# Kernel tuning notes

Hardware: AMD Instinct MI355X
Metric: run time of the kernel (lower is better)

## Reference

```python
import jax, jax.numpy as jnp
import numpy as np

Q_INTERVAL = 4          # opt.interval
Q = 2 ** Q_INTERVAL     # 16, quantization bin width
L = 2 ** (8 - Q_INTERVAL) + 1  # 17, LUT side length
OUT_C = 3
BD = 1                  # padding for mode 's'


def setup_inputs() -> dict:
    key = jax.random.key(0)
    k_img, k_w = jax.random.split(key)
    # 8-bit pixel values stored as float32 (the torch module does // and % on floats)
    img_in = jax.random.randint(k_img, (8, 1, 513, 513), 0, 256).astype(jnp.float32)
    # LUT parameter, stored as float in [-1, 1] (npy / 127.0 in the original)
    weight = jax.random.uniform(k_w, (L ** 4, OUT_C), dtype=jnp.float32,
                                minval=-1.0, maxval=1.0)
    return {"img_in": img_in, "weight": weight}


def _interp_s(img_in, weight):
    """Mode 's' quadrilinear (4-simplex) LUT interpolation, faithful to
    SWF2LUT.InterpTorchBatch. The 24 explicit permutation cases in the torch
    code are exactly the descending sort of the four fractional parts
    (ties broken toward the later pixel: d before c before b before a)."""
    # weight quantization: round to int levels in [-127, 127]
    w = jnp.clip(jnp.round(weight * 127.0), -127.0, 127.0)

    h = img_in.shape[2] - BD
    ww = img_in.shape[3] - BD
    # 2x2 neighborhood (mode 's')
    a = img_in[:, :, 0:h,     0:ww]
    b = img_in[:, :, 0:h,     1:1 + ww]
    c = img_in[:, :, 1:1 + h, 0:ww]
    d = img_in[:, :, 1:1 + h, 1:1 + ww]

    ia = jnp.floor_divide(a, Q).astype(jnp.int32)
    ib = jnp.floor_divide(b, Q).astype(jnp.int32)
    ic = jnp.floor_divide(c, Q).astype(jnp.int32)
    idd = jnp.floor_divide(d, Q).astype(jnp.int32)

    f = jnp.stack([a % Q, b % Q, c % Q, d % Q], axis=-1)  # (B,C,h,w,4)

    # Descending sort with ties broken so that larger index (d,c,b,a) comes
    # first -- matches the strict '>' case ordering of the torch code.
    tie_key = f * 4.0 + jnp.arange(4, dtype=f.dtype)
    order = jnp.argsort(-tie_key, axis=-1)                 # (B,C,h,w,4)
    fs = jnp.take_along_axis(f, order, axis=-1)            # sorted desc

    strides = jnp.array([L ** 3, L ** 2, L, 1], dtype=jnp.int32)
    base = ia * (L ** 3) + ib * (L ** 2) + ic * L + idd    # (B,C,h,w)
    sstrides = strides[order]                              # (B,C,h,w,4)
    cum = jnp.cumsum(sstrides, axis=-1)
    # 5 simplex vertices: base, then incrementally add strides in sort order
    idx = jnp.concatenate([base[..., None], base[..., None] + cum], axis=-1)

    p = w[idx]                                             # (B,C,h,w,5,outC)
    wts = jnp.stack([Q - fs[..., 0],
                     fs[..., 0] - fs[..., 1],
                     fs[..., 1] - fs[..., 2],
                     fs[..., 2] - fs[..., 3],
                     fs[..., 3]], axis=-1)                 # (B,C,h,w,5)
    out = jnp.sum(wts[..., None] * p, axis=-2) / Q         # (B,C,h,w,outC)
    return out


def reference(img_in, weight):
    return _interp_s(img_in, weight)
```

## Files before the change

kernel.cpp:

```cpp
#include <hip/hip_runtime.h>
#include <stdint.h>


#define LQ   17
#define L2C  (17 * 17)
#define L3C  (17 * 17 * 17)
#define NENT (L3C * 17)
#define PLANE_STRIDE 83584
#define LDS_BYTES 83584
#define SUMSTRIDE (L3C + L2C + LQ + 1)

__device__ __forceinline__ int stride_of(int j) {
    return j == 0 ? L3C : (j == 1 ? L2C : (j == 2 ? LQ : 1));
}

__global__ __launch_bounds__(256) void quant_planar_kernel(
    const float* __restrict__ w, char* __restrict__ planes, int n) {
    int e = blockIdx.x * 256 + threadIdx.x;
    if (e >= n) return;
#pragma unroll
    for (int ch = 0; ch < 3; ++ch) {
        int q = (int)rintf(w[e * 3 + ch] * 127.0f);
        q = min(127, max(-127, q));
        planes[ch * PLANE_STRIDE + e] = (char)q;
    }
}

extern __shared__ char lut[];

__global__ __launch_bounds__(1024) void interp_fused_kernel(
    const float* __restrict__ img, const char* __restrict__ planes,
    float* __restrict__ out) {
    int G = blockIdx.x * 1024 + threadIdx.x;
    int x0 = (G & 127) << 2;
    int y  = (G >> 7) & 511;
    int im = G >> 16;

    const float* r0 = img + im * (513 * 513) + y * 513 + x0;
    const float* r1 = r0 + 513;
    float v0[5], v1[5];
#pragma unroll
    for (int i = 0; i < 5; ++i) { v0[i] = r0[i]; v1[i] = r1[i]; }

    int pi0[4], pi1[4], pi2[4], pi3[4], pfs[4];
#pragma unroll
    for (int i = 0; i < 4; ++i) {
        int a = (int)v0[i], b = (int)v0[i + 1];
        int c = (int)v1[i], d = (int)v1[i + 1];
        int base = (a >> 4) * L3C + (b >> 4) * L2C + (c >> 4) * LQ + (d >> 4);
        int k0 = ((a & 15) << 2) | 0;
        int k1 = ((b & 15) << 2) | 1;
        int k2 = ((c & 15) << 2) | 2;
        int k3 = ((d & 15) << 2) | 3;
        int t;
        if (k0 < k1) { t = k0; k0 = k1; k1 = t; }
        if (k2 < k3) { t = k2; k2 = k3; k3 = t; }
        if (k0 < k2) { t = k0; k0 = k2; k2 = t; }
        if (k1 < k3) { t = k1; k1 = k3; k3 = t; }
        if (k1 < k2) { t = k1; k1 = k2; k2 = t; }
        int fs0 = k0 >> 2, fs1 = k1 >> 2, fs2 = k2 >> 2, fs3 = k3 >> 2;
        int s0 = stride_of(k0 & 3);
        int s1 = stride_of(k1 & 3);
        int s2 = stride_of(k2 & 3);
        pi0[i] = base;
        pi1[i] = base + s0;
        pi2[i] = base + s0 + s1;
        pi3[i] = base + s0 + s1 + s2;
        pfs[i] = (fs0 << 12) | (fs1 << 8) | (fs2 << 4) | fs3;
    }

    float res[12];
#pragma unroll
    for (int ch = 0; ch < 3; ++ch) {
        __syncthreads();
        {
            const uint4* src =
                (const uint4*)(planes + (size_t)ch * PLANE_STRIDE);
            uint4* dst = (uint4*)lut;
            for (int k = threadIdx.x; k < PLANE_STRIDE / 16; k += 1024)
                dst[k] = src[k];
        }
        __syncthreads();
        const signed char* t8 = (const signed char*)lut;
#pragma unroll
        for (int i = 0; i < 4; ++i) {
            int fs = pfs[i];
            int fs0 = (fs >> 12) & 15, fs1 = (fs >> 8) & 15;
            int fs2 = (fs >> 4) & 15,  fs3 = fs & 15;
            int p0 = t8[pi0[i]];
            int p1 = t8[pi1[i]];
            int p2 = t8[pi2[i]];
            int p3 = t8[pi3[i]];
            int p4 = t8[pi0[i] + SUMSTRIDE];
            int acc = (16 - fs0) * p0 + (fs0 - fs1) * p1 + (fs1 - fs2) * p2 +
                      (fs2 - fs3) * p3 + fs3 * p4;
            res[i * 3 + ch] = (float)acc * 0.0625f;
        }
    }

    int opix = ((im * 512 + y) * 512 + x0) * 3;
    float4* o = (float4*)(out + opix);
    o[0] = make_float4(res[0], res[1], res[2], res[3]);
    o[1] = make_float4(res[4], res[5], res[6], res[7]);
    o[2] = make_float4(res[8], res[9], res[10], res[11]);
}

__global__ __launch_bounds__(256) void quant_pack_kernel(
    const float* __restrict__ w, uint32_t* __restrict__ tab, int n) {
    int e = blockIdx.x * 256 + threadIdx.x;
    if (e >= n) return;
    int q0 = (int)rintf(w[e * 3 + 0] * 127.0f);
    int q1 = (int)rintf(w[e * 3 + 1] * 127.0f);
    int q2 = (int)rintf(w[e * 3 + 2] * 127.0f);
    q0 = min(127, max(-127, q0));
    q1 = min(127, max(-127, q1));
    q2 = min(127, max(-127, q2));
    tab[e] = (uint32_t)(q0 & 0xFF) | ((uint32_t)(q1 & 0xFF) << 8) |
             ((uint32_t)(q2 & 0xFF) << 16);
}

__global__ __launch_bounds__(256) void interp_packed_kernel(
    const float* __restrict__ img, const uint32_t* __restrict__ tab,
    float* __restrict__ out) {
    int gid = blockIdx.x * 256 + threadIdx.x;
    int x0 = (gid & 127) << 2;
    int y  = (gid >> 7) & 511;
    int im = gid >> 16;

    const float* r0 = img + im * (513 * 513) + y * 513 + x0;
    const float* r1 = r0 + 513;
    float v0[5], v1[5];
#pragma unroll
    for (int i = 0; i < 5; ++i) { v0[i] = r0[i]; v1[i] = r1[i]; }

    float res[12];
#pragma unroll
    for (int i = 0; i < 4; ++i) {
        int a = (int)v0[i], b = (int)v0[i + 1];
        int c = (int)v1[i], d = (int)v1[i + 1];
        int base = (a >> 4) * L3C + (b >> 4) * L2C + (c >> 4) * LQ + (d >> 4);
        int k0 = ((a & 15) << 2) | 0;
        int k1 = ((b & 15) << 2) | 1;
        int k2 = ((c & 15) << 2) | 2;
        int k3 = ((d & 15) << 2) | 3;
        int t;
        if (k0 < k1) { t = k0; k0 = k1; k1 = t; }
        if (k2 < k3) { t = k2; k2 = k3; k3 = t; }
        if (k0 < k2) { t = k0; k0 = k2; k2 = t; }
        if (k1 < k3) { t = k1; k1 = k3; k3 = t; }
        if (k1 < k2) { t = k1; k1 = k2; k2 = t; }
        int fs0 = k0 >> 2, fs1 = k1 >> 2, fs2 = k2 >> 2, fs3 = k3 >> 2;
        int s0 = stride_of(k0 & 3);
        int s1 = stride_of(k1 & 3);
        int s2 = stride_of(k2 & 3);
        int i0 = base;
        int i1 = base + s0;
        int i2 = i1 + s1;
        int i3 = i2 + s2;
        int i4 = base + SUMSTRIDE;
        uint32_t u0 = tab[i0], u1 = tab[i1], u2 = tab[i2], u3 = tab[i3],
                 u4 = tab[i4];
        int w0 = 16 - fs0, w1 = fs0 - fs1, w2 = fs1 - fs2, w3 = fs2 - fs3,
            w4 = fs3;
#pragma unroll
        for (int chn = 0; chn < 3; ++chn) {
            int sh = 24 - chn * 8;
            int p0 = (int)(u0 << sh) >> 24;
            int p1 = (int)(u1 << sh) >> 24;
            int p2 = (int)(u2 << sh) >> 24;
            int p3 = (int)(u3 << sh) >> 24;
            int p4 = (int)(u4 << sh) >> 24;
            int acc = w0 * p0 + w1 * p1 + w2 * p2 + w3 * p3 + w4 * p4;
            res[i * 3 + chn] = (float)acc * 0.0625f;
        }
    }

    int opix = ((im * 512 + y) * 512 + x0) * 3;
    float4* o = (float4*)(out + opix);
    o[0] = make_float4(res[0], res[1], res[2], res[3]);
    o[1] = make_float4(res[4], res[5], res[6], res[7]);
    o[2] = make_float4(res[8], res[9], res[10], res[11]);
}

extern "C" void kernel_launch(void* const* d_in, const int* in_sizes, int n_in,
                              void* d_out, int out_size, void* d_ws,
                              size_t ws_size, hipStream_t stream) {
    const float* img = (const float*)d_in[0];
    const float* wgt = (const float*)d_in[1];
    float* out = (float*)d_out;

    const size_t planes_bytes = (size_t)3 * PLANE_STRIDE;

    bool lds_ok = (ws_size >= planes_bytes) && (d_ws != nullptr);
    if (lds_ok) {
        hipError_t e = hipFuncSetAttribute(
            reinterpret_cast<const void*>(interp_fused_kernel),
            hipFuncAttributeMaxDynamicSharedMemorySize, LDS_BYTES);
        lds_ok = (e == hipSuccess);
    }

    if (lds_ok) {
        char* planes = (char*)d_ws;
        quant_planar_kernel<<<(NENT + 255) / 256, 256, 0, stream>>>(
            wgt, planes, NENT);
        interp_fused_kernel<<<512, 1024, LDS_BYTES, stream>>>(img, planes,
                                                              out);
    } else if (ws_size >= (size_t)NENT * sizeof(uint32_t) && d_ws != nullptr) {
        uint32_t* tab = (uint32_t*)d_ws;
        quant_pack_kernel<<<(NENT + 255) / 256, 256, 0, stream>>>(wgt, tab,
                                                                  NENT);
        interp_packed_kernel<<<8 * 512 * 128 / 256, 256, 0, stream>>>(
            img, tab, out);
    }
}
```

Measured before the change: 36.36 us.

## Process eight pixels per thread to halve LUT plane staging in fused kernel

Each thread now computes eight output pixels instead of four, so the grid shrinks from 512 to 256 blocks. Every block copies the three 83 KB LUT planes into LDS, so this halves the total global-to-LDS staging traffic. Per-pixel vertex offsets and per-channel accumulators are bit-packed to keep register use down under the 1024-thread launch bound. The cost is more registers per thread and only 256 blocks, which may leave compute units underused or cause spills.

```diff
diff --git a/kernel.cpp b/kernel.cpp
--- a/kernel.cpp
+++ b/kernel.cpp
@@ -7,7 +7,7 @@
 #define L3C  (17 * 17 * 17)
 #define NENT (L3C * 17)
 #define PLANE_STRIDE 83584
-#define LDS_BYTES 83584
+#define LDS_BYTES   83584
 #define SUMSTRIDE (L3C + L2C + LQ + 1)
 
 __device__ __forceinline__ int stride_of(int j) {
@@ -32,19 +32,19 @@
     const float* __restrict__ img, const char* __restrict__ planes,
     float* __restrict__ out) {
     int G = blockIdx.x * 1024 + threadIdx.x;
-    int x0 = (G & 127) << 2;
-    int y  = (G >> 7) & 511;
-    int im = G >> 16;
+    int x0 = (G & 63) << 3;
+    int y  = (G >> 6) & 511;
+    int im = G >> 15;
 
     const float* r0 = img + im * (513 * 513) + y * 513 + x0;
     const float* r1 = r0 + 513;
-    float v0[5], v1[5];
-#pragma unroll
-    for (int i = 0; i < 5; ++i) { v0[i] = r0[i]; v1[i] = r1[i]; }
-
-    int pi0[4], pi1[4], pi2[4], pi3[4], pfs[4];
-#pragma unroll
-    for (int i = 0; i < 4; ++i) {
+    float v0[9], v1[9];
+#pragma unroll
+    for (int i = 0; i < 9; ++i) { v0[i] = r0[i]; v1[i] = r1[i]; }
+
+    int pi0[8], pk1[8], pk2[8];
+#pragma unroll
+    for (int i = 0; i < 8; ++i) {
         int a = (int)v0[i], b = (int)v0[i + 1];
         int c = (int)v1[i], d = (int)v1[i + 1];
         int base = (a >> 4) * L3C + (b >> 4) * L2C + (c >> 4) * LQ + (d >> 4);
@@ -60,16 +60,19 @@
         if (k1 < k2) { t = k1; k1 = k2; k2 = t; }
         int fs0 = k0 >> 2, fs1 = k1 >> 2, fs2 = k2 >> 2, fs3 = k3 >> 2;
         int s0 = stride_of(k0 & 3);
-        int s1 = stride_of(k1 & 3);
-        int s2 = stride_of(k2 & 3);
+        int s01 = s0 + stride_of(k1 & 3);
+        int s012 = s01 + stride_of(k2 & 3);
         pi0[i] = base;
-        pi1[i] = base + s0;
-        pi2[i] = base + s0 + s1;
-        pi3[i] = base + s0 + s1 + s2;
-        pfs[i] = (fs0 << 12) | (fs1 << 8) | (fs2 << 4) | fs3;
-    }
-
-    float res[12];
+        pk1[i] = s0 | (s01 << 13);
+        pk2[i] = (fs0 << 12) | (fs1 << 8) | (fs2 << 4) | fs3 | (s012 << 16);
+    }
+
+    int racc[3][4];
+#pragma unroll
+    for (int ch = 0; ch < 3; ++ch)
+#pragma unroll
+        for (int p = 0; p < 4; ++p) racc[ch][p] = 0;
+
 #pragma unroll
     for (int ch = 0; ch < 3; ++ch) {
         __syncthreads();
@@ -83,26 +86,43 @@
         __syncthreads();
         const signed char* t8 = (const signed char*)lut;
 #pragma unroll
-        for (int i = 0; i < 4; ++i) {
-            int fs = pfs[i];
+        for (int i = 0; i < 8; ++i) {
+            int fs = pk2[i];
             int fs0 = (fs >> 12) & 15, fs1 = (fs >> 8) & 15;
             int fs2 = (fs >> 4) & 15,  fs3 = fs & 15;
-            int p0 = t8[pi0[i]];
-            int p1 = t8[pi1[i]];
-            int p2 = t8[pi2[i]];
-            int p3 = t8[pi3[i]];
-            int p4 = t8[pi0[i] + SUMSTRIDE];
+            int i0 = pi0[i];
+            int i1 = i0 + (pk1[i] & 0x1FFF);
+            int i2 = i0 + (pk1[i] >> 13);
+            int i3 = i0 + ((fs >> 16) & 0x1FFF);
+            int i4 = i0 + SUMSTRIDE;
+            int p0 = t8[i0];
+            int p1 = t8[i1];
+            int p2 = t8[i2];
+            int p3 = t8[i3];
+            int p4 = t8[i4];
             int acc = (16 - fs0) * p0 + (fs0 - fs1) * p1 + (fs1 - fs2) * p2 +
                       (fs2 - fs3) * p3 + fs3 * p4;
-            res[i * 3 + ch] = (float)acc * 0.0625f;
-        }
-    }
+            racc[ch][i >> 1] |= (acc & 0xFFFF) << (16 * (i & 1));
+        }
+    }
+
+    float res[24];
+#pragma unroll
+    for (int ch = 0; ch < 3; ++ch)
+#pragma unroll
+        for (int p = 0; p < 4; ++p) {
+            int lo = (racc[ch][p] << 16) >> 16;
+            int hi = racc[ch][p] >> 16;
+            res[(2 * p) * 3 + ch]     = (float)lo * 0.0625f;
+            res[(2 * p + 1) * 3 + ch] = (float)hi * 0.0625f;
+        }
 
     int opix = ((im * 512 + y) * 512 + x0) * 3;
     float4* o = (float4*)(out + opix);
-    o[0] = make_float4(res[0], res[1], res[2], res[3]);
-    o[1] = make_float4(res[4], res[5], res[6], res[7]);
-    o[2] = make_float4(res[8], res[9], res[10], res[11]);
+#pragma unroll
+    for (int q = 0; q < 6; ++q)
+        o[q] = make_float4(res[q * 4], res[q * 4 + 1], res[q * 4 + 2],
+                           res[q * 4 + 3]);
 }
 
 __global__ __launch_bounds__(256) void quant_pack_kernel(
@@ -203,7 +223,7 @@
         char* planes = (char*)d_ws;
         quant_planar_kernel<<<(NENT + 255) / 256, 256, 0, stream>>>(
             wgt, planes, NENT);
-        interp_fused_kernel<<<512, 1024, LDS_BYTES, stream>>>(img, planes,
+        interp_fused_kernel<<<256, 1024, LDS_BYTES, stream>>>(img, planes,
                                                               out);
     } else if (ws_size >= (size_t)NENT * sizeof(uint32_t) && d_ws != nullptr) {
         uint32_t* tab = (uint32_t*)d_ws;
```

New measurement: 36.43 us. About the same (+0.2%).
